# Kernel optimization log

Measured on AMD Instinct MI355X. Metric: run time of the kernel, lower is better.

Reference implementation:

```python
import jax, jax.numpy as jnp
import numpy as np

V, NB, NJ, NP, NK = 6890, 10, 24, 207, 19
PARENTS = np.array([-1, 0, 0, 0, 1, 2, 3, 4, 5, 6, 7, 8, 9, 9, 9, 12, 13, 14, 16, 17, 18, 19, 20, 21])


def setup_inputs():
    key = jax.random.key(0)
    ks = jax.random.split(key, 9)
    B = 1024
    beta = jax.random.normal(ks[0], (B, NB), jnp.float32)
    theta = jax.random.normal(ks[1], (B, NJ * 3), jnp.float32) * 0.3  # axis-angle per joint
    trans = jax.random.normal(ks[2], (B, 3), jnp.float32)
    v_template = jax.random.normal(ks[3], (V, 3), jnp.float32)
    shapedirs = jax.random.normal(ks[4], (NB, V * 3), jnp.float32) * 0.03
    Jr = jax.random.uniform(ks[5], (V, NJ), jnp.float32)
    J_regressor = Jr / jnp.sum(Jr, axis=0, keepdims=True)
    posedirs = jax.random.normal(ks[6], (NP, V * 3), jnp.float32) * 0.01
    jr = jax.random.uniform(ks[7], (V, NK), jnp.float32)
    joint_regressor = jr / jnp.sum(jr, axis=0, keepdims=True)
    w = jax.random.uniform(ks[8], (V, NJ), jnp.float32)
    weights = w / jnp.sum(w, axis=1, keepdims=True)  # LBS weights, rows sum to 1
    return dict(beta=beta, theta=theta, trans=trans, v_template=v_template,
                shapedirs=shapedirs, J_regressor=J_regressor, posedirs=posedirs,
                joint_regressor=joint_regressor, weights=weights)


def batch_rodrigues(theta):
    # theta: (N,3) axis-angle -> (N,3,3) rotation matrices via quaternions (HMR-style)
    angle = jnp.linalg.norm(theta + 1e-8, axis=1, keepdims=True)
    half = angle * 0.5
    v = (theta / angle) * jnp.sin(half)
    quat = jnp.concatenate([jnp.cos(half), v], axis=1)
    quat = quat / jnp.linalg.norm(quat, axis=1, keepdims=True)
    w, x, y, z = quat[:, 0], quat[:, 1], quat[:, 2], quat[:, 3]
    rot = jnp.stack([
        1 - 2 * (y * y + z * z), 2 * (x * y - w * z), 2 * (x * z + w * y),
        2 * (x * y + w * z), 1 - 2 * (x * x + z * z), 2 * (y * z - w * x),
        2 * (x * z - w * y), 2 * (y * z + w * x), 1 - 2 * (x * x + y * y)], axis=1)
    return rot.reshape(-1, 3, 3)


def batch_global_rigid_transformation(Rs, J):
    # Rs: (B,24,3,3), J: (B,24,3); rotate_base=True
    B = Rs.shape[0]
    rot_x = jnp.array([[1., 0., 0.], [0., -1., 0.], [0., 0., -1.]], jnp.float32)
    root_R = Rs[:, 0] @ rot_x

    def make_A(R, t):  # (B,3,3),(B,3) -> (B,4,4)
        top = jnp.concatenate([R, t[:, :, None]], axis=2)
        bot = jnp.broadcast_to(jnp.array([0., 0., 0., 1.], jnp.float32), (B, 1, 4))
        return jnp.concatenate([top, bot], axis=1)

    results = [make_A(root_R, J[:, 0])]
    for i in range(1, NJ):  # fixed 24-joint kinematic chain
        t = J[:, i] - J[:, PARENTS[i]]
        results.append(results[PARENTS[i]] @ make_A(Rs[:, i], t))
    res = jnp.stack(results, axis=1)  # (B,24,4,4)
    new_J = res[:, :, :3, 3]
    j_w0 = jnp.concatenate([J, jnp.zeros_like(J[:, :, :1])], axis=2)  # (B,24,4), homo w=0
    init_bone = jnp.einsum('bjrc,bjc->bjr', res, j_w0)
    A = res.at[:, :, :, 3].add(-init_bone)  # subtract only last column (matches F.pad trick)
    return new_J, A


def reference(beta, theta, trans, v_template, shapedirs, J_regressor, posedirs, joint_regressor, weights):
    B = beta.shape[0]
    v_shaped = (beta @ shapedirs).reshape(B, V, 3) + v_template
    J = jnp.einsum('bvc,vj->bjc', v_shaped, J_regressor)  # (B,24,3)
    Rs = batch_rodrigues(theta.reshape(-1, 3)).reshape(B, NJ, 3, 3)
    pose_feature = (Rs[:, 1:] - jnp.eye(3, dtype=Rs.dtype)).reshape(B, NP)
    v_posed = (pose_feature @ posedirs).reshape(B, V, 3) + v_shaped
    _, A = batch_global_rigid_transformation(Rs, J)
    T = jnp.einsum('vj,bjrc->bvrc', weights, A)  # (B,V,4,4) per-vertex skinning transforms
    homo = jnp.concatenate([v_posed, jnp.ones((B, V, 1), v_posed.dtype)], axis=2)
    verts = jnp.einsum('bvrc,bvc->bvr', T, homo)[:, :, :3] + trans[:, None, :]
    joints = jnp.einsum('bvc,vk->bkc', verts, joint_regressor)  # (B,19,3)
    return joints
```

## Files before the change

kernel.cpp:

```cpp
#include <hip/hip_runtime.h>
#include <hip/hip_bf16.h>

constexpr int Vn   = 6890;
constexpr int VC3  = 20670;
constexpr int NKB  = 216;
constexpr int QT   = 224;
constexpr int NMG  = 14;
constexpr int NCOL = 480;
constexpr int MC   = 1368;
constexpr int KCH  = 27;

using bf16x8  = __attribute__((ext_vector_type(8))) short;
using floatx4 = __attribute__((ext_vector_type(4))) float;

__device__ __forceinline__ unsigned short f2bf(float f) {
    unsigned int u = __float_as_uint(f);
    unsigned int r = (u + 0x7FFFu + ((u >> 16) & 1u)) >> 16;
    return (unsigned short)r;
}

__global__ __launch_bounds__(256) void k0_build(
    const float* __restrict__ vt, const float* __restrict__ sdirs,
    const float* __restrict__ pdirs, const float* __restrict__ Jreg,
    const float* __restrict__ jreg, const float* __restrict__ wts,
    const float* __restrict__ beta, const float* __restrict__ theta,
    unsigned short* __restrict__ Af, unsigned short* __restrict__ Bf,
    float* __restrict__ Rsg, unsigned short* __restrict__ xbf)
{
    __shared__ float smem[16 * 385];
    int bx = blockIdx.x, t = threadIdx.x;
    if (bx < 756) {
        int mg = bx / 54, ub = bx % 54;
        int fbase = ub * 384;
        for (int i = t; i < 16 * 384; i += 256) {
            int qr = i / 384, off = i % 384;
            int q = mg * 16 + qr;
            int gidx = fbase + off;
            float v = 0.f;
            if (q == 0) v = (gidx < VC3) ? 1.f : 0.f;
            else {
                const float* src = nullptr;
                if (q == 1) src = vt;
                else if (q < 12)  src = sdirs + (size_t)(q - 2) * VC3;
                else if (q < 219) src = pdirs + (size_t)(q - 12) * VC3;
                if (src && gidx < VC3) v = src[gidx];
            }
            smem[qr * 385 + off] = v;
        }
        __syncthreads();
        int ql = t & 15, uul = t >> 4;
        int uu = ub * 16 + uul;
        int kb = uu >> 2, quad = uu & 3;
        size_t foff = (size_t)(ql + quad * 16) * 8;
        const float* lrow = smem + ql * 385 + uul * 24;
        #pragma unroll
        for (int c = 0; c < 3; ++c) {
            bf16x8 o;
            #pragma unroll
            for (int j = 0; j < 8; ++j) o[j] = (short)f2bf(lrow[3 * j + c]);
            *(bf16x8*)(Af + ((size_t)(c * NMG + mg) * NKB + kb) * 512 + foff) = o;
        }
        return;
    }
    bx -= 756;
    if (bx < 108) {
        int v0 = bx * 64;
        float* js  = smem;
        float* wsh = smem + 1216;
        float* Jsh = smem + 2752;
        for (int i = t; i < 64 * 19; i += 256)
            js[i] = (v0 * 19 + i < Vn * 19) ? jreg[v0 * 19 + i] : 0.f;
        for (int i = t; i < 64 * 24; i += 256) {
            wsh[i] = (v0 * 24 + i < Vn * 24) ? wts[v0 * 24 + i] : 0.f;
            Jsh[i] = (v0 * 24 + i < Vn * 24) ? Jreg[v0 * 24 + i] : 0.f;
        }
        __syncthreads();
        for (int s = t; s < 4096; s += 256) {
            int clow = s & 15, w = s >> 4;
            int vg = w & 7, chigh = w >> 3;
            int col = chigh * 16 + clow;
            int kb = (v0 >> 5) + (vg >> 2);
            bf16x8 o;
            #pragma unroll
            for (int j = 0; j < 8; ++j) {
                int vl = vg * 8 + j;
                float val = 0.f;
                if (col < 456)      val = js[vl * 19 + col / 24] * wsh[vl * 24 + col % 24];
                else if (col < 480) val = Jsh[vl * 24 + (col - 456)];
                o[j] = (short)f2bf(val);
            }
            *(bf16x8*)(Bf + ((size_t)chigh * NKB + kb) * 512
                          + (size_t)(clow + (vg & 3) * 16) * 8) = o;
        }
        return;
    }
    bx -= 108;
    {
        float (*Rc)[24][9] = (float(*)[24][9])smem;
        int b0 = bx * 16;
        for (int i = t; i < 384; i += 256) {
            int bl = i / 24, j = i % 24;
            float t0 = theta[(size_t)(b0 + bl) * 72 + j * 3 + 0];
            float t1 = theta[(size_t)(b0 + bl) * 72 + j * 3 + 1];
            float t2 = theta[(size_t)(b0 + bl) * 72 + j * 3 + 2];
            float e0 = t0 + 1e-8f, e1 = t1 + 1e-8f, e2 = t2 + 1e-8f;
            float angle = sqrtf(e0 * e0 + e1 * e1 + e2 * e2);
            float half = 0.5f * angle;
            float sh = sinf(half), ch = cosf(half);
            float s = sh / angle;
            float qx = t0 * s, qy = t1 * s, qz = t2 * s;
            float qn = sqrtf(ch * ch + qx * qx + qy * qy + qz * qz);
            float w = ch / qn, x = qx / qn, y = qy / qn, z = qz / qn;
            float r0 = 1.f - 2.f * (y * y + z * z);
            float r1 = 2.f * (x * y - w * z);
            float r2 = 2.f * (x * z + w * y);
            float r3 = 2.f * (x * y + w * z);
            float r4 = 1.f - 2.f * (x * x + z * z);
            float r5 = 2.f * (y * z - w * x);
            float r6 = 2.f * (x * z - w * y);
            float r7 = 2.f * (y * z + w * x);
            float r8 = 1.f - 2.f * (x * x + y * y);
            Rc[bl][j][0] = r0; Rc[bl][j][1] = r1; Rc[bl][j][2] = r2;
            Rc[bl][j][3] = r3; Rc[bl][j][4] = r4; Rc[bl][j][5] = r5;
            Rc[bl][j][6] = r6; Rc[bl][j][7] = r7; Rc[bl][j][8] = r8;
            float* rg = Rsg + (size_t)(b0 + bl) * 216 + j * 9;
            rg[0] = r0; rg[1] = r1; rg[2] = r2;
            rg[3] = r3; rg[4] = r4; rg[5] = r5;
            rg[6] = r6; rg[7] = r7; rg[8] = r8;
        }
        __syncthreads();
        for (int i = t; i < 16 * QT; i += 256) {
            int q = i >> 4, bl = i & 15;
            int b = b0 + bl;
            float xv = 0.f;
            if (q == 1) xv = 1.f;
            else if (q >= 2 && q < 12) xv = beta[(size_t)b * 10 + (q - 2)];
            else if (q >= 12 && q < 219) {
                int p = q - 12;
                int jj = 1 + p / 9, e = p % 9;
                float rr = Rc[bl][jj][e];
                if (e == 0 || e == 4 || e == 8) rr -= 1.f;
                xv = rr;
            }
            xbf[((size_t)(b >> 4) * 7 + (q >> 5)) * 512
                + (size_t)((b & 15) + ((q >> 3) & 3) * 16) * 8 + (q & 7)] = f2bf(xv);
        }
    }
}

__device__ __forceinline__ void k1_load(bf16x8 (&a)[2], bf16x8 (&b)[4],
    const unsigned short* __restrict__ ap, const unsigned short* __restrict__ bp, int i)
{
    a[0] = *(const bf16x8*)(ap + (size_t)(0 * NKB + i) * 512);
    a[1] = *(const bf16x8*)(ap + (size_t)(1 * NKB + i) * 512);
    b[0] = *(const bf16x8*)(bp + (size_t)(0 * NKB + i) * 512);
    b[1] = *(const bf16x8*)(bp + (size_t)(1 * NKB + i) * 512);
    b[2] = *(const bf16x8*)(bp + (size_t)(2 * NKB + i) * 512);
    b[3] = *(const bf16x8*)(bp + (size_t)(3 * NKB + i) * 512);
}

__global__ __launch_bounds__(512) void k1_mfma(
    const unsigned short* __restrict__ Af, const unsigned short* __restrict__ Bf,
    unsigned short* __restrict__ Wb3, float* __restrict__ w1g,
    float* __restrict__ Jacc)
{
    __shared__ float red[8 * 2048];
    int tid = threadIdx.x;
    int wv = tid >> 6, l = tid & 63;
    int r = blockIdx.x;
    int c = r / 56; r %= 56;
    int mt = r >> 3, nt = r & 7;
    int kb0 = wv * KCH;

    const unsigned short* ap = Af + ((size_t)(c * NMG + mt * 2) * NKB + kb0) * 512 + l * 8;
    const unsigned short* bp = Bf + ((size_t)(nt * 4) * NKB + kb0) * 512 + l * 8;

    floatx4 acc[2][4];
    #pragma unroll
    for (int mi = 0; mi < 2; ++mi)
        #pragma unroll
        for (int ni = 0; ni < 4; ++ni) acc[mi][ni] = floatx4{0.f, 0.f, 0.f, 0.f};

    bf16x8 a[3][2], b[3][4];
    k1_load(a[0], b[0], ap, bp, 0);
    k1_load(a[1], b[1], ap, bp, 1);
    #pragma unroll
    for (int i = 0; i < KCH; ++i) {
        if (i + 2 < KCH) k1_load(a[(i + 2) % 3], b[(i + 2) % 3], ap, bp, i + 2);
        bf16x8 (&ac)[2] = a[i % 3];
        bf16x8 (&bc)[4] = b[i % 3];
        #pragma unroll
        for (int mi = 0; mi < 2; ++mi)
            #pragma unroll
            for (int ni = 0; ni < 4; ++ni)
                acc[mi][ni] = __builtin_amdgcn_mfma_f32_16x16x32_bf16(ac[mi], bc[ni], acc[mi][ni], 0, 0, 0);
    }
    #pragma unroll
    for (int mi = 0; mi < 2; ++mi)
        #pragma unroll
        for (int ni = 0; ni < 4; ++ni)
            *(floatx4*)&red[wv * 2048 + ((mi * 4 + ni) * 64 + l) * 4] = acc[mi][ni];
    __syncthreads();
    if (tid < 256) {
        int cl = tid & 63, qo = tid >> 6;
        int ni = cl >> 4;
        int q0 = qo * 8;
        int li0 = ((q0 & 15) >> 2) * 16 + (cl & 15);
        int li1 = (((q0 + 4) & 15) >> 2) * 16 + (cl & 15);
        int base0 = (((q0 >> 4) * 4 + ni) * 64 + li0) * 4;
        int base1 = ((((q0 + 4) >> 4) * 4 + ni) * 64 + li1) * 4;
        floatx4 s0{0.f, 0.f, 0.f, 0.f}, s1{0.f, 0.f, 0.f, 0.f};
        #pragma unroll
        for (int ww = 0; ww < 8; ++ww) {
            s0 += *(const floatx4*)&red[ww * 2048 + base0];
            s1 += *(const floatx4*)&red[ww * 2048 + base1];
        }
        int col = nt * 64 + cl;
        if (col < NCOL) {
            int colc = col * 3 + c;
            if (colc < MC) {
                bf16x8 o;
                #pragma unroll
                for (int j = 0; j < 4; ++j) {
                    o[j]     = (short)f2bf(s0[j]);
                    o[4 + j] = (short)f2bf(s1[j]);
                }
                *(bf16x8*)(Wb3 + ((size_t)(colc >> 4) * 7 + mt) * 512
                               + (size_t)((colc & 15) + qo * 16) * 8) = o;
            }
            if (c == 0 && mt == 0 && qo == 0 && col < 456) w1g[col] = s0[0];
            if (mt == 0 && col >= 456) {
                float* jb = Jacc + (size_t)((col - 456) * 3 + c) * 11;
                if (qo == 0) {
                    jb[0] = s0[1]; jb[1] = s0[2]; jb[2] = s0[3];
                    jb[3] = s1[0]; jb[4] = s1[1]; jb[5] = s1[2]; jb[6] = s1[3];
                } else if (qo == 1) {
                    jb[7] = s0[0]; jb[8] = s0[1]; jb[9] = s0[2]; jb[10] = s0[3];
                }
            }
        }
    }
}

__global__ __launch_bounds__(512) void k2_tail(
    const unsigned short* __restrict__ Wb3, const unsigned short* __restrict__ xbf,
    const float* __restrict__ Rsg, const float* __restrict__ Jacc,
    const float* __restrict__ w1g, const float* __restrict__ beta,
    const float* __restrict__ trans, float* __restrict__ out)
{
    __shared__ float Rs[16][24][9];
    __shared__ float Jl[16][24][3];
    __shared__ float resR[16][24][9];
    __shared__ float rest_[16][24][3];
    __shared__ float Msh[16][145];
    int t = threadIdx.x;
    int bt = blockIdx.x / 10, kp = blockIdx.x % 10;
    int b0 = bt * 16;
    int nmg = (kp == 9) ? 5 : 9;
    int mgbase = kp * 9;

    for (int i = t; i < 3456; i += 512)
        ((float*)Rs)[i] = Rsg[(size_t)b0 * 216 + i];
    for (int i = t; i < 1152; i += 512) {
        int bl = i / 72, jc = i % 72;
        const float* bp_ = Jacc + (size_t)jc * 11;
        const float* be  = beta + (size_t)(b0 + bl) * 10;
        float a = bp_[0];
        #pragma unroll
        for (int n = 0; n < 10; ++n) a += be[n] * bp_[1 + n];
        Jl[bl][jc / 3][jc % 3] = a;
    }
    __syncthreads();
    int wv = t >> 6, l = t & 63;
    if (wv == 0) {
        if (l < 48) {
            const int par[24] = {-1,0,0,0,1,2,3,4,5,6,7,8,9,9,9,12,13,14,16,17,18,19,20,21};
            int bl = l / 3, rr = l % 3;
            resR[bl][0][rr * 3 + 0] =  Rs[bl][0][rr * 3 + 0];
            resR[bl][0][rr * 3 + 1] = -Rs[bl][0][rr * 3 + 1];
            resR[bl][0][rr * 3 + 2] = -Rs[bl][0][rr * 3 + 2];
            rest_[bl][0][rr] = Jl[bl][0][rr];
            for (int i = 1; i < 24; ++i) {
                int p = par[i];
                float t0 = Jl[bl][i][0] - Jl[bl][p][0];
                float t1 = Jl[bl][i][1] - Jl[bl][p][1];
                float t2 = Jl[bl][i][2] - Jl[bl][p][2];
                float a0 = resR[bl][p][rr * 3 + 0], a1 = resR[bl][p][rr * 3 + 1],
                      a2 = resR[bl][p][rr * 3 + 2];
                resR[bl][i][rr * 3 + 0] = a0 * Rs[bl][i][0] + a1 * Rs[bl][i][3] + a2 * Rs[bl][i][6];
                resR[bl][i][rr * 3 + 1] = a0 * Rs[bl][i][1] + a1 * Rs[bl][i][4] + a2 * Rs[bl][i][7];
                resR[bl][i][rr * 3 + 2] = a0 * Rs[bl][i][2] + a1 * Rs[bl][i][5] + a2 * Rs[bl][i][8];
                rest_[bl][i][rr] = a0 * t0 + a1 * t1 + a2 * t2 + rest_[bl][p][rr];
            }
        }
    } else {
        const unsigned short* bp = xbf + (size_t)bt * 7 * 512 + l * 8;
        for (int mgl = wv - 1; mgl < nmg; mgl += 7) {
            const unsigned short* ap = Wb3 + (size_t)(mgbase + mgl) * 7 * 512 + l * 8;
            floatx4 acc{0.f, 0.f, 0.f, 0.f};
            #pragma unroll
            for (int kk = 0; kk < 7; ++kk)
                acc = __builtin_amdgcn_mfma_f32_16x16x32_bf16(
                    *(const bf16x8*)(ap + (size_t)kk * 512),
                    *(const bf16x8*)(bp + (size_t)kk * 512), acc, 0, 0, 0);
            int bl = l & 15, cc0 = mgl * 16 + (l >> 4) * 4;
            #pragma unroll
            for (int rr = 0; rr < 4; ++rr) Msh[bl][cc0 + rr] = acc[rr];
        }
    }
    __syncthreads();
    int nk = (kp == 9) ? 1 : 2;
    for (int i = t; i < 48 * nk; i += 512) {
        int kl = i / 48, r2 = i % 48;
        int bl = r2 / 3, c = r2 % 3;
        int b = b0 + bl, k = kp * 2 + kl;
        float s = trans[b * 3 + c];
        const float* mrow = Msh[bl] + kl * 72;
        const float* w1k  = w1g + k * 24;
        #pragma unroll
        for (int j = 0; j < 24; ++j) {
            float ta = rest_[bl][j][c]
                - (resR[bl][j][c * 3 + 0] * Jl[bl][j][0]
                 + resR[bl][j][c * 3 + 1] * Jl[bl][j][1]
                 + resR[bl][j][c * 3 + 2] * Jl[bl][j][2]);
            s += ta * w1k[j];
            s += resR[bl][j][c * 3 + 0] * mrow[j * 3 + 0]
               + resR[bl][j][c * 3 + 1] * mrow[j * 3 + 1]
               + resR[bl][j][c * 3 + 2] * mrow[j * 3 + 2];
        }
        out[(size_t)b * 57 + k * 3 + c] = s;
    }
}

extern "C" void kernel_launch(void* const* d_in, const int* in_sizes, int n_in,
                              void* d_out, int out_size, void* d_ws, size_t ws_size,
                              hipStream_t stream)
{
    const float* beta  = (const float*)d_in[0];
    const float* theta = (const float*)d_in[1];
    const float* trans = (const float*)d_in[2];
    const float* vt    = (const float*)d_in[3];
    const float* sdirs = (const float*)d_in[4];
    const float* Jreg  = (const float*)d_in[5];
    const float* pdirs = (const float*)d_in[6];
    const float* jreg  = (const float*)d_in[7];
    const float* wts   = (const float*)d_in[8];
    float* out = (float*)d_out;
    int B = in_sizes[0] / 10;

    unsigned short* Af  = (unsigned short*)d_ws;
    unsigned short* Bf  = Af + (size_t)42 * NKB * 512;
    unsigned short* Wb3 = Bf + (size_t)32 * NKB * 512;
    unsigned short* xbf = Wb3 + (size_t)88 * 7 * 512;
    float* Jacc = (float*)(xbf + (size_t)64 * 7 * 512);
    float* w1g  = Jacc + 792;
    float* Rsg  = w1g + 456;

    k0_build<<<dim3(756 + 108 + 64), 256, 0, stream>>>(
        vt, sdirs, pdirs, Jreg, jreg, wts, beta, theta, Af, Bf, Rsg, xbf);
    k1_mfma<<<dim3(168), 512, 0, stream>>>(Af, Bf, Wb3, w1g, Jacc);
    k2_tail<<<dim3((B / 16) * 10), 512, 0, stream>>>(
        Wb3, xbf, Rsg, Jacc, w1g, beta, trans, out);
}
```

Before: 125.2 us.

## Merge three kernels into one cooperative persistent kernel with grid syncs

```diff
diff --git a/kernel.cpp b/kernel.cpp
--- a/kernel.cpp
+++ b/kernel.cpp
@@ -1,5 +1,8 @@
 #include <hip/hip_runtime.h>
 #include <hip/hip_bf16.h>
+#include <hip/hip_cooperative_groups.h>
+
+namespace cg = cooperative_groups;
 
 constexpr int Vn   = 6890;
 constexpr int VC3  = 20670;
@@ -19,316 +22,325 @@
     return (unsigned short)r;
 }
 
-__global__ __launch_bounds__(256) void k0_build(
+__global__ __launch_bounds__(512) void mega(
     const float* __restrict__ vt, const float* __restrict__ sdirs,
     const float* __restrict__ pdirs, const float* __restrict__ Jreg,
     const float* __restrict__ jreg, const float* __restrict__ wts,
     const float* __restrict__ beta, const float* __restrict__ theta,
+    const float* __restrict__ trans,
     unsigned short* __restrict__ Af, unsigned short* __restrict__ Bf,
-    float* __restrict__ Rsg, unsigned short* __restrict__ xbf)
+    unsigned short* __restrict__ Wb3, unsigned short* __restrict__ xbf,
+    float* __restrict__ Jacc, float* __restrict__ w1g,
+    float* __restrict__ Rsg, float* __restrict__ out)
 {
-    __shared__ float smem[16 * 385];
-    int bx = blockIdx.x, t = threadIdx.x;
-    if (bx < 756) {
-        int mg = bx / 54, ub = bx % 54;
-        int fbase = ub * 384;
-        for (int i = t; i < 16 * 384; i += 256) {
-            int qr = i / 384, off = i % 384;
-            int q = mg * 16 + qr;
-            int gidx = fbase + off;
-            float v = 0.f;
-            if (q == 0) v = (gidx < VC3) ? 1.f : 0.f;
-            else {
-                const float* src = nullptr;
-                if (q == 1) src = vt;
-                else if (q < 12)  src = sdirs + (size_t)(q - 2) * VC3;
-                else if (q < 219) src = pdirs + (size_t)(q - 12) * VC3;
-                if (src && gidx < VC3) v = src[gidx];
-            }
-            smem[qr * 385 + off] = v;
-        }
-        __syncthreads();
-        int ql = t & 15, uul = t >> 4;
-        int uu = ub * 16 + uul;
-        int kb = uu >> 2, quad = uu & 3;
-        size_t foff = (size_t)(ql + quad * 16) * 8;
-        const float* lrow = smem + ql * 385 + uul * 24;
-        #pragma unroll
-        for (int c = 0; c < 3; ++c) {
-            bf16x8 o;
-            #pragma unroll
-            for (int j = 0; j < 8; ++j) o[j] = (short)f2bf(lrow[3 * j + c]);
-            *(bf16x8*)(Af + ((size_t)(c * NMG + mg) * NKB + kb) * 512 + foff) = o;
-        }
-        return;
-    }
-    bx -= 756;
-    if (bx < 108) {
-        int v0 = bx * 64;
-        float* js  = smem;
-        float* wsh = smem + 1216;
-        float* Jsh = smem + 2752;
-        for (int i = t; i < 64 * 19; i += 256)
-            js[i] = (v0 * 19 + i < Vn * 19) ? jreg[v0 * 19 + i] : 0.f;
-        for (int i = t; i < 64 * 24; i += 256) {
-            wsh[i] = (v0 * 24 + i < Vn * 24) ? wts[v0 * 24 + i] : 0.f;
-            Jsh[i] = (v0 * 24 + i < Vn * 24) ? Jreg[v0 * 24 + i] : 0.f;
-        }
-        __syncthreads();
-        for (int s = t; s < 4096; s += 256) {
-            int clow = s & 15, w = s >> 4;
-            int vg = w & 7, chigh = w >> 3;
-            int col = chigh * 16 + clow;
-            int kb = (v0 >> 5) + (vg >> 2);
-            bf16x8 o;
-            #pragma unroll
-            for (int j = 0; j < 8; ++j) {
-                int vl = vg * 8 + j;
-                float val = 0.f;
-                if (col < 456)      val = js[vl * 19 + col / 24] * wsh[vl * 24 + col % 24];
-                else if (col < 480) val = Jsh[vl * 24 + (col - 456)];
-                o[j] = (short)f2bf(val);
-            }
-            *(bf16x8*)(Bf + ((size_t)chigh * NKB + kb) * 512
-                          + (size_t)(clow + (vg & 3) * 16) * 8) = o;
-        }
-        return;
-    }
-    bx -= 108;
+    __shared__ __attribute__((aligned(16))) float smem[16384];
+    cg::grid_group grid = cg::this_grid();
+    const int bid = blockIdx.x;
+    const int t   = threadIdx.x;
+
     {
-        float (*Rc)[24][9] = (float(*)[24][9])smem;
-        int b0 = bx * 16;
-        for (int i = t; i < 384; i += 256) {
-            int bl = i / 24, j = i % 24;
-            float t0 = theta[(size_t)(b0 + bl) * 72 + j * 3 + 0];
-            float t1 = theta[(size_t)(b0 + bl) * 72 + j * 3 + 1];
-            float t2 = theta[(size_t)(b0 + bl) * 72 + j * 3 + 2];
-            float e0 = t0 + 1e-8f, e1 = t1 + 1e-8f, e2 = t2 + 1e-8f;
-            float angle = sqrtf(e0 * e0 + e1 * e1 + e2 * e2);
-            float half = 0.5f * angle;
-            float sh = sinf(half), ch = cosf(half);
-            float s = sh / angle;
-            float qx = t0 * s, qy = t1 * s, qz = t2 * s;
-            float qn = sqrtf(ch * ch + qx * qx + qy * qy + qz * qz);
-            float w = ch / qn, x = qx / qn, y = qy / qn, z = qz / qn;
-            float r0 = 1.f - 2.f * (y * y + z * z);
-            float r1 = 2.f * (x * y - w * z);
-            float r2 = 2.f * (x * z + w * y);
-            float r3 = 2.f * (x * y + w * z);
-            float r4 = 1.f - 2.f * (x * x + z * z);
-            float r5 = 2.f * (y * z - w * x);
-            float r6 = 2.f * (x * z - w * y);
-            float r7 = 2.f * (y * z + w * x);
-            float r8 = 1.f - 2.f * (x * x + y * y);
-            Rc[bl][j][0] = r0; Rc[bl][j][1] = r1; Rc[bl][j][2] = r2;
-            Rc[bl][j][3] = r3; Rc[bl][j][4] = r4; Rc[bl][j][5] = r5;
-            Rc[bl][j][6] = r6; Rc[bl][j][7] = r7; Rc[bl][j][8] = r8;
-            float* rg = Rsg + (size_t)(b0 + bl) * 216 + j * 9;
-            rg[0] = r0; rg[1] = r1; rg[2] = r2;
-            rg[3] = r3; rg[4] = r4; rg[5] = r5;
-            rg[6] = r6; rg[7] = r7; rg[8] = r8;
-        }
-        __syncthreads();
-        for (int i = t; i < 16 * QT; i += 256) {
-            int q = i >> 4, bl = i & 15;
-            int b = b0 + bl;
-            float xv = 0.f;
-            if (q == 1) xv = 1.f;
-            else if (q >= 2 && q < 12) xv = beta[(size_t)b * 10 + (q - 2)];
-            else if (q >= 12 && q < 219) {
-                int p = q - 12;
-                int jj = 1 + p / 9, e = p % 9;
-                float rr = Rc[bl][jj][e];
-                if (e == 0 || e == 4 || e == 8) rr -= 1.f;
-                xv = rr;
-            }
-            xbf[((size_t)(b >> 4) * 7 + (q >> 5)) * 512
-                + (size_t)((b & 15) + ((q >> 3) & 3) * 16) * 8 + (q & 7)] = f2bf(xv);
+        const int ul = t >> 8, tl = t & 255;
+        float* sm = smem + ul * 6160;
+        for (int u = bid * 2 + ul; u < 928; u += 512) {
+            if (u < 756) {
+                int mg = u / 54, ub = u % 54;
+                int fbase = ub * 384;
+                for (int i = tl; i < 16 * 384; i += 256) {
+                    int qr = i / 384, off = i % 384;
+                    int q = mg * 16 + qr;
+                    int gidx = fbase + off;
+                    float v = 0.f;
+                    if (q == 0) v = (gidx < VC3) ? 1.f : 0.f;
+                    else {
+                        const float* src = nullptr;
+                        if (q == 1) src = vt;
+                        else if (q < 12)  src = sdirs + (size_t)(q - 2) * VC3;
+                        else if (q < 219) src = pdirs + (size_t)(q - 12) * VC3;
+                        if (src && gidx < VC3) v = src[gidx];
+                    }
+                    sm[qr * 385 + off] = v;
+                }
+                __syncthreads();
+                int ql = tl & 15, uul = tl >> 4;
+                int uu = ub * 16 + uul;
+                int kb = uu >> 2, quad = uu & 3;
+                size_t foff = (size_t)(ql + quad * 16) * 8;
+                const float* lrow = sm + ql * 385 + uul * 24;
+                #pragma unroll
+                for (int c = 0; c < 3; ++c) {
+                    bf16x8 o;
+                    #pragma unroll
+                    for (int j = 0; j < 8; ++j) o[j] = (short)f2bf(lrow[3 * j + c]);
+                    *(bf16x8*)(Af + ((size_t)(c * NMG + mg) * NKB + kb) * 512 + foff) = o;
+                }
+            } else if (u < 864) {
+                int bx = u - 756;
+                int v0 = bx * 64;
+                float* js  = sm;
+                float* wsh = sm + 1216;
+                float* Jsh = sm + 2752;
+                for (int i = tl; i < 64 * 19; i += 256)
+                    js[i] = (v0 * 19 + i < Vn * 19) ? jreg[v0 * 19 + i] : 0.f;
+                for (int i = tl; i < 64 * 24; i += 256) {
+                    wsh[i] = (v0 * 24 + i < Vn * 24) ? wts[v0 * 24 + i] : 0.f;
+                    Jsh[i] = (v0 * 24 + i < Vn * 24) ? Jreg[v0 * 24 + i] : 0.f;
+                }
+                __syncthreads();
+                for (int s = tl; s < 4096; s += 256) {
+                    int clow = s & 15, w = s >> 4;
+                    int vg = w & 7, chigh = w >> 3;
+                    int col = chigh * 16 + clow;
+                    int kb = (v0 >> 5) + (vg >> 2);
+                    bf16x8 o;
+                    #pragma unroll
+                    for (int j = 0; j < 8; ++j) {
+                        int vl = vg * 8 + j;
+                        float val = 0.f;
+                        if (col < 456)      val = js[vl * 19 + col / 24] * wsh[vl * 24 + col % 24];
+                        else if (col < 480) val = Jsh[vl * 24 + (col - 456)];
+                        o[j] = (short)f2bf(val);
+                    }
+                    *(bf16x8*)(Bf + ((size_t)chigh * NKB + kb) * 512
+                                  + (size_t)(clow + (vg & 3) * 16) * 8) = o;
+                }
+            } else {
+                int bx = u - 864;
+                float (*Rc)[24][9] = (float(*)[24][9])sm;
+                int b0 = bx * 16;
+                for (int i = tl; i < 384; i += 256) {
+                    int bl = i / 24, j = i % 24;
+                    float t0 = theta[(size_t)(b0 + bl) * 72 + j * 3 + 0];
+                    float t1 = theta[(size_t)(b0 + bl) * 72 + j * 3 + 1];
+                    float t2 = theta[(size_t)(b0 + bl) * 72 + j * 3 + 2];
+                    float e0 = t0 + 1e-8f, e1 = t1 + 1e-8f, e2 = t2 + 1e-8f;
+                    float angle = sqrtf(e0 * e0 + e1 * e1 + e2 * e2);
+                    float half = 0.5f * angle;
+                    float sh = sinf(half), ch = cosf(half);
+                    float s = sh / angle;
+                    float qx = t0 * s, qy = t1 * s, qz = t2 * s;
+                    float qn = sqrtf(ch * ch + qx * qx + qy * qy + qz * qz);
+                    float w = ch / qn, x = qx / qn, y = qy / qn, z = qz / qn;
+                    float r0 = 1.f - 2.f * (y * y + z * z);
+                    float r1 = 2.f * (x * y - w * z);
+                    float r2 = 2.f * (x * z + w * y);
+                    float r3 = 2.f * (x * y + w * z);
+                    float r4 = 1.f - 2.f * (x * x + z * z);
+                    float r5 = 2.f * (y * z - w * x);
+                    float r6 = 2.f * (x * z - w * y);
+                    float r7 = 2.f * (y * z + w * x);
+                    float r8 = 1.f - 2.f * (x * x + y * y);
+                    Rc[bl][j][0] = r0; Rc[bl][j][1] = r1; Rc[bl][j][2] = r2;
+                    Rc[bl][j][3] = r3; Rc[bl][j][4] = r4; Rc[bl][j][5] = r5;
+                    Rc[bl][j][6] = r6; Rc[bl][j][7] = r7; Rc[bl][j][8] = r8;
+                    float* rg = Rsg + (size_t)(b0 + bl) * 216 + j * 9;
+                    rg[0] = r0; rg[1] = r1; rg[2] = r2;
+                    rg[3] = r3; rg[4] = r4; rg[5] = r5;
+                    rg[6] = r6; rg[7] = r7; rg[8] = r8;
+                }
+                __syncthreads();
+                for (int i = tl; i < 16 * QT; i += 256) {
+                    int q = i >> 4, bl = i & 15;
+                    int b = b0 + bl;
+                    float xv = 0.f;
+                    if (q == 1) xv = 1.f;
+                    else if (q >= 2 && q < 12) xv = beta[(size_t)b * 10 + (q - 2)];
+                    else if (q >= 12 && q < 219) {
+                        int p = q - 12;
+                        int jj = 1 + p / 9, e = p % 9;
+                        float rr = Rc[bl][jj][e];
+                        if (e == 0 || e == 4 || e == 8) rr -= 1.f;
+                        xv = rr;
+                    }
+                    xbf[((size_t)(b >> 4) * 7 + (q >> 5)) * 512
+                        + (size_t)((b & 15) + ((q >> 3) & 3) * 16) * 8 + (q & 7)] = f2bf(xv);
+                }
+            }
+            __syncthreads();
         }
     }
-}
-
-__device__ __forceinline__ void k1_load(bf16x8 (&a)[2], bf16x8 (&b)[4],
-    const unsigned short* __restrict__ ap, const unsigned short* __restrict__ bp, int i)
-{
-    a[0] = *(const bf16x8*)(ap + (size_t)(0 * NKB + i) * 512);
-    a[1] = *(const bf16x8*)(ap + (size_t)(1 * NKB + i) * 512);
-    b[0] = *(const bf16x8*)(bp + (size_t)(0 * NKB + i) * 512);
-    b[1] = *(const bf16x8*)(bp + (size_t)(1 * NKB + i) * 512);
-    b[2] = *(const bf16x8*)(bp + (size_t)(2 * NKB + i) * 512);
-    b[3] = *(const bf16x8*)(bp + (size_t)(3 * NKB + i) * 512);
-}
-
-__global__ __launch_bounds__(512) void k1_mfma(
-    const unsigned short* __restrict__ Af, const unsigned short* __restrict__ Bf,
-    unsigned short* __restrict__ Wb3, float* __restrict__ w1g,
-    float* __restrict__ Jacc)
-{
-    __shared__ float red[8 * 2048];
-    int tid = threadIdx.x;
-    int wv = tid >> 6, l = tid & 63;
-    int r = blockIdx.x;
-    int c = r / 56; r %= 56;
-    int mt = r >> 3, nt = r & 7;
-    int kb0 = wv * KCH;
-
-    const unsigned short* ap = Af + ((size_t)(c * NMG + mt * 2) * NKB + kb0) * 512 + l * 8;
-    const unsigned short* bp = Bf + ((size_t)(nt * 4) * NKB + kb0) * 512 + l * 8;
-
-    floatx4 acc[2][4];
-    #pragma unroll
-    for (int mi = 0; mi < 2; ++mi)
+    grid.sync();
+    if (bid < 168) {
+        float* red = smem;
+        const int tid = t;
+        int wv = tid >> 6, l = tid & 63;
+        int r = bid;
+        int c = r / 56; r %= 56;
+        int mt = r >> 3, nt = r & 7;
+        int kb0 = wv * KCH;
+
+        const unsigned short* ap = Af + ((size_t)(c * NMG + mt * 2) * NKB + kb0) * 512 + l * 8;
+        const unsigned short* bp = Bf + ((size_t)(nt * 4) * NKB + kb0) * 512 + l * 8;
+
+        floatx4 acc[2][4];
         #pragma unroll
-        for (int ni = 0; ni < 4; ++ni) acc[mi][ni] = floatx4{0.f, 0.f, 0.f, 0.f};
-
-    bf16x8 a[3][2], b[3][4];
-    k1_load(a[0], b[0], ap, bp, 0);
-    k1_load(a[1], b[1], ap, bp, 1);
-    #pragma unroll
-    for (int i = 0; i < KCH; ++i) {
-        if (i + 2 < KCH) k1_load(a[(i + 2) % 3], b[(i + 2) % 3], ap, bp, i + 2);
-        bf16x8 (&ac)[2] = a[i % 3];
-        bf16x8 (&bc)[4] = b[i % 3];
+        for (int mi = 0; mi < 2; ++mi)
+            #pragma unroll
+            for (int ni = 0; ni < 4; ++ni) acc[mi][ni] = floatx4{0.f, 0.f, 0.f, 0.f};
+
+        bf16x8 a[3][2], b[3][4];
+        a[0][0] = *(const bf16x8*)(ap + (size_t)(0 * NKB + 0) * 512);
+        a[0][1] = *(const bf16x8*)(ap + (size_t)(1 * NKB + 0) * 512);
+        b[0][0] = *(const bf16x8*)(bp + (size_t)(0 * NKB + 0) * 512);
+        b[0][1] = *(const bf16x8*)(bp + (size_t)(1 * NKB + 0) * 512);
+        b[0][2] = *(const bf16x8*)(bp + (size_t)(2 * NKB + 0) * 512);
+        b[0][3] = *(const bf16x8*)(bp + (size_t)(3 * NKB + 0) * 512);
+        a[1][0] = *(const bf16x8*)(ap + (size_t)(0 * NKB + 1) * 512);
+        a[1][1] = *(const bf16x8*)(ap + (size_t)(1 * NKB + 1) * 512);
+        b[1][0] = *(const bf16x8*)(bp + (size_t)(0 * NKB + 1) * 512);
+        b[1][1] = *(const bf16x8*)(bp + (size_t)(1 * NKB + 1) * 512);
+        b[1][2] = *(const bf16x8*)(bp + (size_t)(2 * NKB + 1) * 512);
+        b[1][3] = *(const bf16x8*)(bp + (size_t)(3 * NKB + 1) * 512);
+        #pragma unroll
+        for (int i = 0; i < KCH; ++i) {
+            if (i + 2 < KCH) {
+                int nx = (i + 2) % 3;
+                a[nx][0] = *(const bf16x8*)(ap + (size_t)(0 * NKB + i + 2) * 512);
+                a[nx][1] = *(const bf16x8*)(ap + (size_t)(1 * NKB + i + 2) * 512);
+                b[nx][0] = *(const bf16x8*)(bp + (size_t)(0 * NKB + i + 2) * 512);
+                b[nx][1] = *(const bf16x8*)(bp + (size_t)(1 * NKB + i + 2) * 512);
+                b[nx][2] = *(const bf16x8*)(bp + (size_t)(2 * NKB + i + 2) * 512);
+                b[nx][3] = *(const bf16x8*)(bp + (size_t)(3 * NKB + i + 2) * 512);
+            }
+            bf16x8 (&ac)[2] = a[i % 3];
+            bf16x8 (&bc)[4] = b[i % 3];
+            #pragma unroll
+            for (int mi = 0; mi < 2; ++mi)
+                #pragma unroll
+                for (int ni = 0; ni < 4; ++ni)
+                    acc[mi][ni] = __builtin_amdgcn_mfma_f32_16x16x32_bf16(ac[mi], bc[ni], acc[mi][ni], 0, 0, 0);
+        }
         #pragma unroll
         for (int mi = 0; mi < 2; ++mi)
             #pragma unroll
             for (int ni = 0; ni < 4; ++ni)
-                acc[mi][ni] = __builtin_amdgcn_mfma_f32_16x16x32_bf16(ac[mi], bc[ni], acc[mi][ni], 0, 0, 0);
-    }
-    #pragma unroll
-    for (int mi = 0; mi < 2; ++mi)
-        #pragma unroll
-        for (int ni = 0; ni < 4; ++ni)
-            *(floatx4*)&red[wv * 2048 + ((mi * 4 + ni) * 64 + l) * 4] = acc[mi][ni];
-    __syncthreads();
-    if (tid < 256) {
-        int cl = tid & 63, qo = tid >> 6;
-        int ni = cl >> 4;
-        int q0 = qo * 8;
-        int li0 = ((q0 & 15) >> 2) * 16 + (cl & 15);
-        int li1 = (((q0 + 4) & 15) >> 2) * 16 + (cl & 15);
-        int base0 = (((q0 >> 4) * 4 + ni) * 64 + li0) * 4;
-        int base1 = ((((q0 + 4) >> 4) * 4 + ni) * 64 + li1) * 4;
-        floatx4 s0{0.f, 0.f, 0.f, 0.f}, s1{0.f, 0.f, 0.f, 0.f};
-        #pragma unroll
-        for (int ww = 0; ww < 8; ++ww) {
-            s0 += *(const floatx4*)&red[ww * 2048 + base0];
-            s1 += *(const floatx4*)&red[ww * 2048 + base1];
-        }
-        int col = nt * 64 + cl;
-        if (col < NCOL) {
-            int colc = col * 3 + c;
-            if (colc < MC) {
-                bf16x8 o;
-                #pragma unroll
-                for (int j = 0; j < 4; ++j) {
-                    o[j]     = (short)f2bf(s0[j]);
-                    o[4 + j] = (short)f2bf(s1[j]);
-                }
-                *(bf16x8*)(Wb3 + ((size_t)(colc >> 4) * 7 + mt) * 512
-                               + (size_t)((colc & 15) + qo * 16) * 8) = o;
-            }
-            if (c == 0 && mt == 0 && qo == 0 && col < 456) w1g[col] = s0[0];
-            if (mt == 0 && col >= 456) {
-                float* jb = Jacc + (size_t)((col - 456) * 3 + c) * 11;
-                if (qo == 0) {
-                    jb[0] = s0[1]; jb[1] = s0[2]; jb[2] = s0[3];
-                    jb[3] = s1[0]; jb[4] = s1[1]; jb[5] = s1[2]; jb[6] = s1[3];
-                } else if (qo == 1) {
-                    jb[7] = s0[0]; jb[8] = s0[1]; jb[9] = s0[2]; jb[10] = s0[3];
+                *(floatx4*)&red[wv * 2048 + ((mi * 4 + ni) * 64 + l) * 4] = acc[mi][ni];
+        __syncthreads();
+        if (tid < 256) {
+            int cl = tid & 63, qo = tid >> 6;
+            int ni = cl >> 4;
+            int q0 = qo * 8;
+            int li0 = ((q0 & 15) >> 2) * 16 + (cl & 15);
+            int li1 = (((q0 + 4) & 15) >> 2) * 16 + (cl & 15);
+            int base0 = (((q0 >> 4) * 4 + ni) * 64 + li0) * 4;
+            int base1 = ((((q0 + 4) >> 4) * 4 + ni) * 64 + li1) * 4;
+            floatx4 s0{0.f, 0.f, 0.f, 0.f}, s1{0.f, 0.f, 0.f, 0.f};
+            #pragma unroll
+            for (int ww = 0; ww < 8; ++ww) {
+                s0 += *(const floatx4*)&red[ww * 2048 + base0];
+                s1 += *(const floatx4*)&red[ww * 2048 + base1];
+            }
+            int col = nt * 64 + cl;
+            if (col < NCOL) {
+                int colc = col * 3 + c;
+                if (colc < MC) {
+                    bf16x8 o;
+                    #pragma unroll
+                    for (int j = 0; j < 4; ++j) {
+                        o[j]     = (short)f2bf(s0[j]);
+                        o[4 + j] = (short)f2bf(s1[j]);
+                    }
+                    *(bf16x8*)(Wb3 + ((size_t)(colc >> 4) * 7 + mt) * 512
+                                   + (size_t)((colc & 15) + qo * 16) * 8) = o;
+                }
+                if (c == 0 && mt == 0 && qo == 0 && col < 456) w1g[col] = s0[0];
+                if (mt == 0 && col >= 456) {
+                    float* jb = Jacc + (size_t)((col - 456) * 3 + c) * 11;
+                    if (qo == 0) {
+                        jb[0] = s0[1]; jb[1] = s0[2]; jb[2] = s0[3];
+                        jb[3] = s1[0]; jb[4] = s1[1]; jb[5] = s1[2]; jb[6] = s1[3];
+                    } else if (qo == 1) {
+                        jb[7] = s0[0]; jb[8] = s0[1]; jb[9] = s0[2]; jb[10] = s0[3];
+                    }
                 }
             }
         }
     }
-}
-
-__global__ __launch_bounds__(512) void k2_tail(
-    const unsigned short* __restrict__ Wb3, const unsigned short* __restrict__ xbf,
-    const float* __restrict__ Rsg, const float* __restrict__ Jacc,
-    const float* __restrict__ w1g, const float* __restrict__ beta,
-    const float* __restrict__ trans, float* __restrict__ out)
-{
-    __shared__ float Rs[16][24][9];
-    __shared__ float Jl[16][24][3];
-    __shared__ float resR[16][24][9];
-    __shared__ float rest_[16][24][3];
-    __shared__ float Msh[16][145];
-    int t = threadIdx.x;
-    int bt = blockIdx.x / 10, kp = blockIdx.x % 10;
-    int b0 = bt * 16;
-    int nmg = (kp == 9) ? 5 : 9;
-    int mgbase = kp * 9;
-
-    for (int i = t; i < 3456; i += 512)
-        ((float*)Rs)[i] = Rsg[(size_t)b0 * 216 + i];
-    for (int i = t; i < 1152; i += 512) {
-        int bl = i / 72, jc = i % 72;
-        const float* bp_ = Jacc + (size_t)jc * 11;
-        const float* be  = beta + (size_t)(b0 + bl) * 10;
-        float a = bp_[0];
-        #pragma unroll
-        for (int n = 0; n < 10; ++n) a += be[n] * bp_[1 + n];
-        Jl[bl][jc / 3][jc % 3] = a;
-    }
-    __syncthreads();
-    int wv = t >> 6, l = t & 63;
-    if (wv == 0) {
-        if (l < 48) {
-            const int par[24] = {-1,0,0,0,1,2,3,4,5,6,7,8,9,9,9,12,13,14,16,17,18,19,20,21};
-            int bl = l / 3, rr = l % 3;
-            resR[bl][0][rr * 3 + 0] =  Rs[bl][0][rr * 3 + 0];
-            resR[bl][0][rr * 3 + 1] = -Rs[bl][0][rr * 3 + 1];
-            resR[bl][0][rr * 3 + 2] = -Rs[bl][0][rr * 3 + 2];
-            rest_[bl][0][rr] = Jl[bl][0][rr];
-            for (int i = 1; i < 24; ++i) {
-                int p = par[i];
-                float t0 = Jl[bl][i][0] - Jl[bl][p][0];
-                float t1 = Jl[bl][i][1] - Jl[bl][p][1];
-                float t2 = Jl[bl][i][2] - Jl[bl][p][2];
-                float a0 = resR[bl][p][rr * 3 + 0], a1 = resR[bl][p][rr * 3 + 1],
-                      a2 = resR[bl][p][rr * 3 + 2];
-                resR[bl][i][rr * 3 + 0] = a0 * Rs[bl][i][0] + a1 * Rs[bl][i][3] + a2 * Rs[bl][i][6];
-                resR[bl][i][rr * 3 + 1] = a0 * Rs[bl][i][1] + a1 * Rs[bl][i][4] + a2 * Rs[bl][i][7];
-                resR[bl][i][rr * 3 + 2] = a0 * Rs[bl][i][2] + a1 * Rs[bl][i][5] + a2 * Rs[bl][i][8];
-                rest_[bl][i][rr] = a0 * t0 + a1 * t1 + a2 * t2 + rest_[bl][p][rr];
-            }
+    grid.sync();
+    {
+        float (*Rs)[24][9]   = (float(*)[24][9])(smem);
+        float (*Jl)[24][3]   = (float(*)[24][3])(smem + 3456);
+        float (*resR)[24][9] = (float(*)[24][9])(smem + 4608);
+        float (*rest_)[24][3]= (float(*)[24][3])(smem + 8064);
+        float* Msh           = smem + 9216;
+        for (int v = bid; v < 640; v += 256) {
+            int bt = v / 10, kp = v % 10;
+            int b0 = bt * 16;
+            int nmg = (kp == 9) ? 5 : 9;
+            int mgbase = kp * 9;
+
+            for (int i = t; i < 3456; i += 512)
+                ((float*)Rs)[i] = Rsg[(size_t)b0 * 216 + i];
+            for (int i = t; i < 1152; i += 512) {
+                int bl = i / 72, jc = i % 72;
+                const float* bp_ = Jacc + (size_t)jc * 11;
+                const float* be  = beta + (size_t)(b0 + bl) * 10;
+                float a = bp_[0];
+                #pragma unroll
+                for (int n = 0; n < 10; ++n) a += be[n] * bp_[1 + n];
+                Jl[bl][jc / 3][jc % 3] = a;
+            }
+            __syncthreads();
+            int wv = t >> 6, l = t & 63;
+            if (wv == 0) {
+                if (l < 48) {
+                    const int par[24] = {-1,0,0,0,1,2,3,4,5,6,7,8,9,9,9,12,13,14,16,17,18,19,20,21};
+                    int bl = l / 3, rr = l % 3;
+                    resR[bl][0][rr * 3 + 0] =  Rs[bl][0][rr * 3 + 0];
+                    resR[bl][0][rr * 3 + 1] = -Rs[bl][0][rr * 3 + 1];
+                    resR[bl][0][rr * 3 + 2] = -Rs[bl][0][rr * 3 + 2];
+                    rest_[bl][0][rr] = Jl[bl][0][rr];
+                    for (int i = 1; i < 24; ++i) {
+                        int p = par[i];
+                        float t0 = Jl[bl][i][0] - Jl[bl][p][0];
+                        float t1 = Jl[bl][i][1] - Jl[bl][p][1];
+                        float t2 = Jl[bl][i][2] - Jl[bl][p][2];
+                        float a0 = resR[bl][p][rr * 3 + 0], a1 = resR[bl][p][rr * 3 + 1],
+                              a2 = resR[bl][p][rr * 3 + 2];
+                        resR[bl][i][rr * 3 + 0] = a0 * Rs[bl][i][0] + a1 * Rs[bl][i][3] + a2 * Rs[bl][i][6];
+                        resR[bl][i][rr * 3 + 1] = a0 * Rs[bl][i][1] + a1 * Rs[bl][i][4] + a2 * Rs[bl][i][7];
+                        resR[bl][i][rr * 3 + 2] = a0 * Rs[bl][i][2] + a1 * Rs[bl][i][5] + a2 * Rs[bl][i][8];
+                        rest_[bl][i][rr] = a0 * t0 + a1 * t1 + a2 * t2 + rest_[bl][p][rr];
+                    }
+                }
+            } else {
+                const unsigned short* bp = xbf + (size_t)bt * 7 * 512 + l * 8;
+                for (int mgl = wv - 1; mgl < nmg; mgl += 7) {
+                    const unsigned short* ap = Wb3 + (size_t)(mgbase + mgl) * 7 * 512 + l * 8;
+                    floatx4 acc{0.f, 0.f, 0.f, 0.f};
+                    #pragma unroll
+                    for (int kk = 0; kk < 7; ++kk)
+                        acc = __builtin_amdgcn_mfma_f32_16x16x32_bf16(
+                            *(const bf16x8*)(ap + (size_t)kk * 512),
+                            *(const bf16x8*)(bp + (size_t)kk * 512), acc, 0, 0, 0);
+                    int bl = l & 15, cc0 = mgl * 16 + (l >> 4) * 4;
+                    #pragma unroll
+                    for (int rr = 0; rr < 4; ++rr) Msh[bl * 145 + cc0 + rr] = acc[rr];
+                }
+            }
+            __syncthreads();
+            int nk = (kp == 9) ? 1 : 2;
+            for (int i = t; i < 48 * nk; i += 512) {
+                int kl = i / 48, r2 = i % 48;
+                int bl = r2 / 3, c = r2 % 3;
+                int b = b0 + bl, k = kp * 2 + kl;
+                float s = trans[b * 3 + c];
+                const float* mrow = Msh + bl * 145 + kl * 72;
+                const float* w1k  = w1g + k * 24;
+                #pragma unroll
+                for (int j = 0; j < 24; ++j) {
+                    float ta = rest_[bl][j][c]
+                        - (resR[bl][j][c * 3 + 0] * Jl[bl][j][0]
+                         + resR[bl][j][c * 3 + 1] * Jl[bl][j][1]
+                         + resR[bl][j][c * 3 + 2] * Jl[bl][j][2]);
+                    s += ta * w1k[j];
+                    s += resR[bl][j][c * 3 + 0] * mrow[j * 3 + 0]
+                       + resR[bl][j][c * 3 + 1] * mrow[j * 3 + 1]
+                       + resR[bl][j][c * 3 + 2] * mrow[j * 3 + 2];
+                }
+                out[(size_t)b * 57 + k * 3 + c] = s;
+            }
+            __syncthreads();
         }
-    } else {
-        const unsigned short* bp = xbf + (size_t)bt * 7 * 512 + l * 8;
-        for (int mgl = wv - 1; mgl < nmg; mgl += 7) {
-            const unsigned short* ap = Wb3 + (size_t)(mgbase + mgl) * 7 * 512 + l * 8;
-            floatx4 acc{0.f, 0.f, 0.f, 0.f};
-            #pragma unroll
-            for (int kk = 0; kk < 7; ++kk)
-                acc = __builtin_amdgcn_mfma_f32_16x16x32_bf16(
-                    *(const bf16x8*)(ap + (size_t)kk * 512),
-                    *(const bf16x8*)(bp + (size_t)kk * 512), acc, 0, 0, 0);
-            int bl = l & 15, cc0 = mgl * 16 + (l >> 4) * 4;
-            #pragma unroll
-            for (int rr = 0; rr < 4; ++rr) Msh[bl][cc0 + rr] = acc[rr];
-        }
-    }
-    __syncthreads();
-    int nk = (kp == 9) ? 1 : 2;
-    for (int i = t; i < 48 * nk; i += 512) {
-        int kl = i / 48, r2 = i % 48;
-        int bl = r2 / 3, c = r2 % 3;
-        int b = b0 + bl, k = kp * 2 + kl;
-        float s = trans[b * 3 + c];
-        const float* mrow = Msh[bl] + kl * 72;
-        const float* w1k  = w1g + k * 24;
-        #pragma unroll
-        for (int j = 0; j < 24; ++j) {
-            float ta = rest_[bl][j][c]
-                - (resR[bl][j][c * 3 + 0] * Jl[bl][j][0]
-                 + resR[bl][j][c * 3 + 1] * Jl[bl][j][1]
-                 + resR[bl][j][c * 3 + 2] * Jl[bl][j][2]);
-            s += ta * w1k[j];
-            s += resR[bl][j][c * 3 + 0] * mrow[j * 3 + 0]
-               + resR[bl][j][c * 3 + 1] * mrow[j * 3 + 1]
-               + resR[bl][j][c * 3 + 2] * mrow[j * 3 + 2];
-        }
-        out[(size_t)b * 57 + k * 3 + c] = s;
     }
 }
 
@@ -347,6 +359,7 @@
     const float* wts   = (const float*)d_in[8];
     float* out = (float*)d_out;
     int B = in_sizes[0] / 10;
+    (void)B;
 
     unsigned short* Af  = (unsigned short*)d_ws;
     unsigned short* Bf  = Af + (size_t)42 * NKB * 512;
@@ -356,9 +369,11 @@
     float* w1g  = Jacc + 792;
     float* Rsg  = w1g + 456;
 
-    k0_build<<<dim3(756 + 108 + 64), 256, 0, stream>>>(
-        vt, sdirs, pdirs, Jreg, jreg, wts, beta, theta, Af, Bf, Rsg, xbf);
-    k1_mfma<<<dim3(168), 512, 0, stream>>>(Af, Bf, Wb3, w1g, Jacc);
-    k2_tail<<<dim3((B / 16) * 10), 512, 0, stream>>>(
-        Wb3, xbf, Rsg, Jacc, w1g, beta, trans, out);
+    void* args[] = {
+        (void*)&vt, (void*)&sdirs, (void*)&pdirs, (void*)&Jreg, (void*)&jreg,
+        (void*)&wts, (void*)&beta, (void*)&theta, (void*)&trans,
+        (void*)&Af, (void*)&Bf, (void*)&Wb3, (void*)&xbf,
+        (void*)&Jacc, (void*)&w1g, (void*)&Rsg, (void*)&out
+    };
+    hipLaunchCooperativeKernel((void*)mega, dim3(256), dim3(512), args, 0, stream);
 }
```

Result: slower. 236.8 us (+89.1%).
